# Optimization experiments

Measured on AMD Instinct MI355X. Metric: run time of the kernel, lower is better.

## Reference

```python
import jax, jax.numpy as jnp
import numpy as np

WIN = 4
HEAD_DIM = 32
N_HEADS = 6
TYPE = 'SW'
SHIFT = WIN // 2  # window_size // 2


def _relation():
    # [P, P, 3] relative coordinate indices into the (2w-1)^3 bias table
    cord = np.array([[i, j, k] for i in range(WIN) for j in range(WIN) for k in range(WIN)])
    return cord[:, None, :] - cord[None, :, :] + WIN - 1


def _shift_mask(nw):
    # boolean mask [nw^3, P, P]; True -> -inf (cross-boundary pairs in shifted windows)
    p, s = WIN, WIN - SHIFT
    m = np.zeros((nw, nw, nw, p, p, p, p, p, p), dtype=bool)
    m[-1, :, :, :s, :, :, s:, :, :] = True
    m[-1, :, :, s:, :, :, :s, :, :] = True
    m[:, -1, :, :, :s, :, :, s:, :] = True
    m[:, -1, :, :, s:, :, :, :s, :] = True
    m[:, :, -1, :, :, :s, :, :, s:] = True
    m[:, :, -1, :, :, s:, :, :, :s] = True
    return m.reshape(nw ** 3, p ** 3, p ** 3)


def setup_inputs() -> dict:
    key = jax.random.key(0)
    ks = jax.random.split(key, 6)
    dim = N_HEADS * HEAD_DIM  # 192
    B, S = 2, 32
    x = jax.random.normal(ks[0], (B, S, S, S, dim), jnp.float32)
    W_qkv = jax.random.normal(ks[1], (dim, 3 * dim), jnp.float32) * 0.02
    b_qkv = jnp.zeros((3 * dim,), jnp.float32)
    rel_params = jax.random.normal(ks[2], (N_HEADS, 2 * WIN - 1, 2 * WIN - 1, 2 * WIN - 1), jnp.float32) * 0.02
    W_out = jax.random.normal(ks[3], (dim, dim), jnp.float32) * 0.02
    b_out = jnp.zeros((dim,), jnp.float32)
    return {"x": x, "W_qkv": W_qkv, "b_qkv": b_qkv, "rel_params": rel_params, "W_out": W_out, "b_out": b_out}


def reference(x, W_qkv, b_qkv, rel_params, W_out, b_out):
    B, H, Wd, D, C = x.shape
    p = WIN
    nw = H // p
    scale = HEAD_DIM ** -0.5
    if TYPE != 'W':
        x = jnp.roll(x, (-SHIFT, -SHIFT, -SHIFT), axis=(1, 2, 3))
    # window partition: [B, NW, P, C], NW = nw^3, P = p^3
    xw = x.reshape(B, nw, p, nw, p, nw, p, C).transpose(0, 1, 3, 5, 2, 4, 6, 7).reshape(B, nw ** 3, p ** 3, C)
    qkv = xw @ W_qkv + b_qkv  # [B, NW, P, 3C]
    qkv = qkv.reshape(B, nw ** 3, p ** 3, 3 * N_HEADS, HEAD_DIM).transpose(3, 0, 1, 2, 4)  # [3h, B, NW, P, d]
    q, k, v = qkv[:N_HEADS], qkv[N_HEADS:2 * N_HEADS], qkv[2 * N_HEADS:]
    sim = jnp.einsum('hbwpc,hbwqc->hbwpq', q, k) * scale
    rel = _relation()
    bias = rel_params[:, rel[:, :, 0], rel[:, :, 1], rel[:, :, 2]]  # [h, P, P]
    sim = sim + bias[:, None, None, :, :]
    if TYPE != 'W':
        mask = jnp.asarray(_shift_mask(nw))[None, None]  # [1,1,NW,P,P]
        sim = jnp.where(mask, -jnp.inf, sim)
    probs = jax.nn.softmax(sim, axis=-1)
    out = jnp.einsum('hbwpq,hbwqc->hbwpc', probs, v)
    out = out.transpose(1, 2, 3, 0, 4).reshape(B, nw ** 3, p ** 3, C)  # h b w p c -> b w p (h c)
    out = out @ W_out + b_out
    out = out.reshape(B, nw, nw, nw, p, p, p, C).transpose(0, 1, 4, 2, 5, 3, 6, 7).reshape(B, H, Wd, D, C)
    if TYPE != 'W':
        out = jnp.roll(out, (SHIFT, SHIFT, SHIFT), axis=(1, 2, 3))
    return out
```

## Files before the change

### kernel.cpp

```cpp
#include <hip/hip_runtime.h>

typedef short bf16x8 __attribute__((ext_vector_type(8)));
typedef float f32x4 __attribute__((ext_vector_type(4)));
typedef unsigned short us4 __attribute__((ext_vector_type(4)));

#define MFMA16(a, b, c) __builtin_amdgcn_mfma_f32_16x16x32_bf16(a, b, c, 0, 0, 0)

__device__ __forceinline__ unsigned short f2bf(float f) {
    unsigned int u = __float_as_uint(f);
    u += 0x7FFFu + ((u >> 16) & 1u);
    return (unsigned short)(u >> 16);
}

#define WQT_OFF 0
#define WOT_OFF 221184
#define BQ_OFF  294912

__global__ void prep_kernel(const float* __restrict__ Wqkv,
                            const float* __restrict__ bqkv,
                            const float* __restrict__ Wout,
                            unsigned short* __restrict__ WqT,
                            unsigned short* __restrict__ WoT,
                            float* __restrict__ bq) {
    const float SCALE = 0.17677669529663687f;
    int i = blockIdx.x * 256 + threadIdx.x;
    if (i < 110592) {
        int n = i / 192, c = i - n * 192;
        float v = Wqkv[c * 576 + n];
        if (n < 192) v *= SCALE;
        WqT[i] = f2bf(v);
    } else if (i < 147456) {
        int j = i - 110592;
        int n = j / 192, c = j - n * 192;
        WoT[j] = f2bf(Wout[c * 192 + n]);
    } else if (i < 148032) {
        int n = i - 147456;
        float v = bqkv[n];
        if (n < 192) v *= SCALE;
        bq[n] = v;
    }
}

#define OFF_X   0
#define OFF_P   0
#define OFF_QK  13312
#define OFF_VT  38400
#define OFF_O   52224
#define OFF_RELF 65536
#define SMEM_US 69652

__global__ __launch_bounds__(512, 2) void wmsa_kernel(
    const float* __restrict__ x, const float* __restrict__ rel,
    const float* __restrict__ bout,
    const unsigned short* __restrict__ WqT,
    const unsigned short* __restrict__ WoT,
    const float* __restrict__ bq, float* __restrict__ out) {
    __shared__ __align__(16) unsigned short smem[SMEM_US];
    float* sRel = (float*)&smem[OFF_RELF];

    const int tid = threadIdx.x;
    const int bw = blockIdx.x;
    const int b  = bw >> 9;
    const int w  = bw & 511;
    const int wz = w >> 6, wy = (w >> 3) & 7, wx = w & 7;

    for (int i = tid; i < 2058; i += 512) sRel[i] = rel[i];
    {
        int t = tid >> 3, q8 = tid & 7;
        int tz = t >> 4, ty = (t >> 2) & 3, tx = t & 3;
        int gz = (wz * 4 + tz + 2) & 31;
        int gy = (wy * 4 + ty + 2) & 31;
        int gx = (wx * 4 + tx + 2) & 31;
        const float* xp = x + ((((b * 32 + gz) * 32 + gy) * 32 + gx)) * 192;
#pragma unroll
        for (int k = 0; k < 6; ++k) {
            int c = (q8 << 2) + (k << 5);
            float4 v = *(const float4*)(xp + c);
            us4 pk;
            pk[0] = f2bf(v.x); pk[1] = f2bf(v.y);
            pk[2] = f2bf(v.z); pk[3] = f2bf(v.w);
            *(us4*)&smem[OFF_X + t * 208 + c] = pk;
        }
    }
    __syncthreads();

    const int lane = tid & 63;
    const int wv   = tid >> 6;
    const int g    = lane >> 4;
    const int l15  = lane & 15;

    {
        bf16x8 afr[4][6];
#pragma unroll
        for (int m = 0; m < 4; ++m)
#pragma unroll
            for (int kk = 0; kk < 6; ++kk)
                afr[m][kk] = *(const bf16x8*)&smem[OFF_X + (m * 16 + l15) * 208 + kk * 32 + g * 8];

        int nb = wv;
        float bias = bq[nb * 16 + l15];
        bf16x8 bfr[6];
        {
            const unsigned short* wp = WqT + (nb * 16 + l15) * 192 + g * 8;
#pragma unroll
            for (int kk = 0; kk < 6; ++kk) bfr[kk] = *(const bf16x8*)(wp + kk * 32);
        }
        while (true) {
            int nbN = nb + 8;
            bool more = (nbN < 36);
            bf16x8 bfrN[6];
            float biasN = 0.f;
            if (more) {
                biasN = bq[nbN * 16 + l15];
                const unsigned short* wp = WqT + (nbN * 16 + l15) * 192 + g * 8;
#pragma unroll
                for (int kk = 0; kk < 6; ++kk) bfrN[kk] = *(const bf16x8*)(wp + kk * 32);
            }
            int colg = nb * 16 + l15;
            bool isV = (nb >= 24);
#pragma unroll
            for (int m = 0; m < 4; ++m) {
                f32x4 acc = {bias, bias, bias, bias};
#pragma unroll
                for (int kk = 0; kk < 6; ++kk) acc = MFMA16(afr[m][kk], bfr[kk], acc);
                int row0 = m * 16 + g * 4;
                if (!isV) {
#pragma unroll
                    for (int r = 0; r < 4; ++r)
                        smem[OFF_QK + (row0 + r) * 392 + colg] = f2bf(acc[r]);
                } else {
                    us4 pk;
#pragma unroll
                    for (int r = 0; r < 4; ++r) pk[r] = f2bf(acc[r]);
                    *(us4*)&smem[OFF_VT + (colg - 384) * 72 + row0] = pk;
                }
            }
            if (!more) break;
            nb = nbN;
            bias = biasN;
#pragma unroll
            for (int kk = 0; kk < 6; ++kk) bfr[kk] = bfrN[kk];
        }
    }
    __syncthreads();

    const bool sz = (wz == 7), sy = (wy == 7), sx = (wx == 7);
    {
        const int qy = (l15 >> 2) & 3, qx = l15 & 3;
        for (int it = wv * 3; it < wv * 3 + 3; ++it) {
            int h = it >> 2, mb = it & 3;
            bf16x8 qf = *(const bf16x8*)&smem[OFF_QK + (mb * 16 + l15) * 392 + h * 32 + g * 8];
            f32x4 s[4];
#pragma unroll
            for (int f = 0; f < 4; ++f) {
                bf16x8 kf = *(const bf16x8*)&smem[OFF_QK + (f * 16 + l15) * 392 + 192 + h * 32 + g * 8];
                f32x4 z = {0.f, 0.f, 0.f, 0.f};
                s[f] = MFMA16(qf, kf, z);
            }
#pragma unroll
            for (int f = 0; f < 4; ++f) {
                bool mz = sz && ((mb < 2) != (f < 2));
                bool my = sy && ((g < 2) != (qy < 2));
                int base = h * 343 + (mb - f + 3) * 49 + (g - qy + 3) * 7 + (3 - qx);
#pragma unroll
                for (int r = 0; r < 4; ++r) {
                    float v = s[f][r] + sRel[base + r];
                    bool mx = sx && ((r < 2) != (qx < 2));
                    s[f][r] = (mz | my | mx) ? -1e30f : v;
                }
            }
#pragma unroll
            for (int r = 0; r < 4; ++r) {
                float m0 = fmaxf(fmaxf(s[0][r], s[1][r]), fmaxf(s[2][r], s[3][r]));
#pragma unroll
                for (int d = 1; d < 16; d <<= 1) m0 = fmaxf(m0, __shfl_xor(m0, d, 64));
                float p0 = __expf(s[0][r] - m0);
                float p1 = __expf(s[1][r] - m0);
                float p2 = __expf(s[2][r] - m0);
                float p3 = __expf(s[3][r] - m0);
                float sm = p0 + p1 + p2 + p3;
#pragma unroll
                for (int d = 1; d < 16; d <<= 1) sm += __shfl_xor(sm, d, 64);
                float inv = 1.0f / sm;
                s[0][r] = p0 * inv; s[1][r] = p1 * inv;
                s[2][r] = p2 * inv; s[3][r] = p3 * inv;
            }
            unsigned short* pbase = &smem[OFF_P + wv * 1152];
#pragma unroll
            for (int f = 0; f < 4; ++f)
#pragma unroll
                for (int r = 0; r < 4; ++r)
                    pbase[(g * 4 + r) * 72 + f * 16 + l15] = f2bf(s[f][r]);
            f32x4 o0 = {0.f, 0.f, 0.f, 0.f}, o1 = {0.f, 0.f, 0.f, 0.f};
#pragma unroll
            for (int kt = 0; kt < 2; ++kt) {
                bf16x8 pf = *(const bf16x8*)&pbase[l15 * 72 + kt * 32 + g * 8];
                bf16x8 v0 = *(const bf16x8*)&smem[OFF_VT + (h * 32 + l15) * 72 + kt * 32 + g * 8];
                bf16x8 v1 = *(const bf16x8*)&smem[OFF_VT + (h * 32 + 16 + l15) * 72 + kt * 32 + g * 8];
                o0 = MFMA16(pf, v0, o0);
                o1 = MFMA16(pf, v1, o1);
            }
#pragma unroll
            for (int r = 0; r < 4; ++r) {
                smem[OFF_O + (mb * 16 + g * 4 + r) * 208 + h * 32 + l15]      = f2bf(o0[r]);
                smem[OFF_O + (mb * 16 + g * 4 + r) * 208 + h * 32 + 16 + l15] = f2bf(o1[r]);
            }
        }
    }
    __syncthreads();

    {
        int mw = wv >> 2, nq = wv & 3;
        bf16x8 ofr[2][6];
#pragma unroll
        for (int mi = 0; mi < 2; ++mi)
#pragma unroll
            for (int kk = 0; kk < 6; ++kk)
                ofr[mi][kk] = *(const bf16x8*)&smem[OFF_O + ((mw * 2 + mi) * 16 + l15) * 208 + kk * 32 + g * 8];
#pragma unroll
        for (int nbi = 0; nbi < 3; ++nbi) {
            int col = (nq + nbi * 4) * 16 + l15;
            float bo = bout[col];
            bf16x8 bfr[6];
            const unsigned short* wp = WoT + col * 192 + g * 8;
#pragma unroll
            for (int kk = 0; kk < 6; ++kk) bfr[kk] = *(const bf16x8*)(wp + kk * 32);
#pragma unroll
            for (int mi = 0; mi < 2; ++mi) {
                f32x4 acc = {bo, bo, bo, bo};
#pragma unroll
                for (int kk = 0; kk < 6; ++kk) acc = MFMA16(ofr[mi][kk], bfr[kk], acc);
                int m = mw * 2 + mi;
                int gz = (wz * 4 + m + 2) & 31;
                int gy = (wy * 4 + g + 2) & 31;
#pragma unroll
                for (int r = 0; r < 4; ++r) {
                    int gx = (wx * 4 + r + 2) & 31;
                    out[(((b * 32 + gz) * 32 + gy) * 32 + gx) * 192 + col] = acc[r];
                }
            }
        }
    }
}

extern "C" void kernel_launch(void* const* d_in, const int* in_sizes, int n_in,
                              void* d_out, int out_size, void* d_ws, size_t ws_size,
                              hipStream_t stream) {
    const float* x    = (const float*)d_in[0];
    const float* Wqkv = (const float*)d_in[1];
    const float* bqkv = (const float*)d_in[2];
    const float* rel  = (const float*)d_in[3];
    const float* Wout = (const float*)d_in[4];
    const float* bout = (const float*)d_in[5];

    unsigned short* WqT = (unsigned short*)((char*)d_ws + WQT_OFF);
    unsigned short* WoT = (unsigned short*)((char*)d_ws + WOT_OFF);
    float*          bq  = (float*)((char*)d_ws + BQ_OFF);
    float*          out = (float*)d_out;

    prep_kernel<<<579, 256, 0, stream>>>(Wqkv, bqkv, Wout, WqT, WoT, bq);
    wmsa_kernel<<<1024, 512, 0, stream>>>(x, rel, bout, WqT, WoT, bq, out);
}
```

Measured before the change: 176.8 us.

## Split attention into per-half-head blocks and move output projection to separate kernel

Each window is now processed by two blocks, each handling three heads with a smaller shared-memory footprint, so more blocks fit per CU. The attention output is written as bf16 to a workspace buffer, and a new oproj_kernel performs the output projection afterwards. The weight prep kernel is also rewritten to use tiled shared-memory transposes for coalesced access. In exchange, each window's x tile is loaded twice and there is an extra global round trip of the attention output plus one more kernel launch.

```diff
diff --git a/kernel.cpp b/kernel.cpp
--- a/kernel.cpp
+++ b/kernel.cpp
@@ -3,6 +3,7 @@
 typedef short bf16x8 __attribute__((ext_vector_type(8)));
 typedef float f32x4 __attribute__((ext_vector_type(4)));
 typedef unsigned short us4 __attribute__((ext_vector_type(4)));
+typedef unsigned short us8 __attribute__((ext_vector_type(8)));
 
 #define MFMA16(a, b, c) __builtin_amdgcn_mfma_f32_16x16x32_bf16(a, b, c, 0, 0, 0)
 
@@ -15,6 +16,7 @@
 #define WQT_OFF 0
 #define WOT_OFF 221184
 #define BQ_OFF  294912
+#define OWS_OFF 297216
 
 __global__ void prep_kernel(const float* __restrict__ Wqkv,
                             const float* __restrict__ bqkv,
@@ -22,65 +24,80 @@
                             unsigned short* __restrict__ WqT,
                             unsigned short* __restrict__ WoT,
                             float* __restrict__ bq) {
+    __shared__ float tile[32][33];
     const float SCALE = 0.17677669529663687f;
-    int i = blockIdx.x * 256 + threadIdx.x;
-    if (i < 110592) {
-        int n = i / 192, c = i - n * 192;
-        float v = Wqkv[c * 576 + n];
-        if (n < 192) v *= SCALE;
-        WqT[i] = f2bf(v);
-    } else if (i < 147456) {
-        int j = i - 110592;
-        int n = j / 192, c = j - n * 192;
-        WoT[j] = f2bf(Wout[c * 192 + n]);
-    } else if (i < 148032) {
-        int n = i - 147456;
-        float v = bqkv[n];
-        if (n < 192) v *= SCALE;
-        bq[n] = v;
-    }
-}
-
-#define OFF_X   0
-#define OFF_P   0
-#define OFF_QK  13312
-#define OFF_VT  38400
-#define OFF_O   52224
-#define OFF_RELF 65536
-#define SMEM_US 69652
-
-__global__ __launch_bounds__(512, 2) void wmsa_kernel(
+    int bid = blockIdx.x;
+    int tx = threadIdx.x & 31, ty = threadIdx.x >> 5;
+    if (bid < 108) {
+        int tn = bid % 18, tc = bid / 18;
+#pragma unroll
+        for (int i = 0; i < 4; ++i)
+            tile[ty + i * 8][tx] = Wqkv[(tc * 32 + ty + i * 8) * 576 + tn * 32 + tx];
+        __syncthreads();
+        bool isQ = (tn < 6);
+#pragma unroll
+        for (int i = 0; i < 4; ++i) {
+            float v = tile[tx][ty + i * 8];
+            if (isQ) v *= SCALE;
+            WqT[(tn * 32 + ty + i * 8) * 192 + tc * 32 + tx] = f2bf(v);
+        }
+    } else if (bid < 144) {
+        int bb = bid - 108;
+        int tn = bb % 6, tc = bb / 6;
+#pragma unroll
+        for (int i = 0; i < 4; ++i)
+            tile[ty + i * 8][tx] = Wout[(tc * 32 + ty + i * 8) * 192 + tn * 32 + tx];
+        __syncthreads();
+#pragma unroll
+        for (int i = 0; i < 4; ++i)
+            WoT[(tn * 32 + ty + i * 8) * 192 + tc * 32 + tx] = f2bf(tile[tx][ty + i * 8]);
+    } else {
+        for (int i = threadIdx.x; i < 576; i += 256) {
+            float v = bqkv[i];
+            if (i < 192) v *= SCALE;
+            bq[i] = v;
+        }
+    }
+}
+
+#define OFF_X    0
+#define OFF_QK   12800
+#define OFF_VT   25600
+#define OFF_RELF 32512
+#define SMEM_US  34570
+
+__global__ __launch_bounds__(384, 3) void wmsa_kernel(
     const float* __restrict__ x, const float* __restrict__ rel,
-    const float* __restrict__ bout,
     const unsigned short* __restrict__ WqT,
-    const unsigned short* __restrict__ WoT,
-    const float* __restrict__ bq, float* __restrict__ out) {
+    const float* __restrict__ bq,
+    unsigned short* __restrict__ Ows) {
     __shared__ __align__(16) unsigned short smem[SMEM_US];
     float* sRel = (float*)&smem[OFF_RELF];
 
     const int tid = threadIdx.x;
-    const int bw = blockIdx.x;
-    const int b  = bw >> 9;
-    const int w  = bw & 511;
+    const int bid = blockIdx.x;
+    const int hh  = bid & 1;
+    const int bw  = bid >> 1;
+    const int b   = bw >> 9;
+    const int w   = bw & 511;
     const int wz = w >> 6, wy = (w >> 3) & 7, wx = w & 7;
 
-    for (int i = tid; i < 2058; i += 512) sRel[i] = rel[i];
-    {
-        int t = tid >> 3, q8 = tid & 7;
+    for (int i = tid; i < 1029; i += 384) sRel[i] = rel[hh * 1029 + i];
+#pragma unroll
+    for (int p = 0; p < 4; ++p) {
+        int f = p * 3072 + tid * 8;
+        int t = f / 192, c = f - t * 192;
         int tz = t >> 4, ty = (t >> 2) & 3, tx = t & 3;
         int gz = (wz * 4 + tz + 2) & 31;
         int gy = (wy * 4 + ty + 2) & 31;
         int gx = (wx * 4 + tx + 2) & 31;
-        const float* xp = x + ((((b * 32 + gz) * 32 + gy) * 32 + gx)) * 192;
-#pragma unroll
-        for (int k = 0; k < 6; ++k) {
-            int c = (q8 << 2) + (k << 5);
-            float4 v = *(const float4*)(xp + c);
-            us4 pk;
-            pk[0] = f2bf(v.x); pk[1] = f2bf(v.y);
-            pk[2] = f2bf(v.z); pk[3] = f2bf(v.w);
-            *(us4*)&smem[OFF_X + t * 208 + c] = pk;
-        }
+        const float* xp = x + ((((b * 32 + gz) * 32 + gy) * 32 + gx)) * 192 + c;
+        float4 v0 = *(const float4*)xp;
+        float4 v1 = *(const float4*)(xp + 4);
+        us8 pk;
+        pk[0] = f2bf(v0.x); pk[1] = f2bf(v0.y); pk[2] = f2bf(v0.z); pk[3] = f2bf(v0.w);
+        pk[4] = f2bf(v1.x); pk[5] = f2bf(v1.y); pk[6] = f2bf(v1.z); pk[7] = f2bf(v1.w);
+        *(us8*)&smem[OFF_X + t * 200 + c] = pk;
     }
     __syncthreads();
 
@@ -89,57 +106,38 @@
     const int g    = lane >> 4;
     const int l15  = lane & 15;
 
-    {
-        bf16x8 afr[4][6];
-#pragma unroll
-        for (int m = 0; m < 4; ++m)
-#pragma unroll
-            for (int kk = 0; kk < 6; ++kk)
-                afr[m][kk] = *(const bf16x8*)&smem[OFF_X + (m * 16 + l15) * 208 + kk * 32 + g * 8];
-
-        int nb = wv;
-        float bias = bq[nb * 16 + l15];
+#pragma unroll
+    for (int j = 0; j < 3; ++j) {
+        int nb = wv + j * 6;
+        int nglob = (nb < 6)  ? (hh * 96 + nb * 16)
+                  : (nb < 12) ? (192 + hh * 96 + (nb - 6) * 16)
+                              : (384 + hh * 96 + (nb - 12) * 16);
+        float bias = bq[nglob + l15];
         bf16x8 bfr[6];
-        {
-            const unsigned short* wp = WqT + (nb * 16 + l15) * 192 + g * 8;
-#pragma unroll
-            for (int kk = 0; kk < 6; ++kk) bfr[kk] = *(const bf16x8*)(wp + kk * 32);
-        }
-        while (true) {
-            int nbN = nb + 8;
-            bool more = (nbN < 36);
-            bf16x8 bfrN[6];
-            float biasN = 0.f;
-            if (more) {
-                biasN = bq[nbN * 16 + l15];
-                const unsigned short* wp = WqT + (nbN * 16 + l15) * 192 + g * 8;
-#pragma unroll
-                for (int kk = 0; kk < 6; ++kk) bfrN[kk] = *(const bf16x8*)(wp + kk * 32);
-            }
-            int colg = nb * 16 + l15;
-            bool isV = (nb >= 24);
-#pragma unroll
-            for (int m = 0; m < 4; ++m) {
-                f32x4 acc = {bias, bias, bias, bias};
-#pragma unroll
-                for (int kk = 0; kk < 6; ++kk) acc = MFMA16(afr[m][kk], bfr[kk], acc);
-                int row0 = m * 16 + g * 4;
-                if (!isV) {
-#pragma unroll
-                    for (int r = 0; r < 4; ++r)
-                        smem[OFF_QK + (row0 + r) * 392 + colg] = f2bf(acc[r]);
-                } else {
-                    us4 pk;
-#pragma unroll
-                    for (int r = 0; r < 4; ++r) pk[r] = f2bf(acc[r]);
-                    *(us4*)&smem[OFF_VT + (colg - 384) * 72 + row0] = pk;
-                }
-            }
-            if (!more) break;
-            nb = nbN;
-            bias = biasN;
-#pragma unroll
-            for (int kk = 0; kk < 6; ++kk) bfr[kk] = bfrN[kk];
+        const unsigned short* wp = WqT + (nglob + l15) * 192 + g * 8;
+#pragma unroll
+        for (int kk = 0; kk < 6; ++kk) bfr[kk] = *(const bf16x8*)(wp + kk * 32);
+#pragma unroll
+        for (int m = 0; m < 4; ++m) {
+            f32x4 acc = {bias, bias, bias, bias};
+#pragma unroll
+            for (int kk = 0; kk < 6; ++kk) {
+                bf16x8 afr = *(const bf16x8*)&smem[OFF_X + (m * 16 + l15) * 200 + kk * 32 + g * 8];
+                acc = MFMA16(afr, bfr[kk], acc);
+            }
+            int row0 = m * 16 + g * 4;
+            if (nb < 12) {
+                int colg = nb * 16 + l15;
+#pragma unroll
+                for (int r = 0; r < 4; ++r)
+                    smem[OFF_QK + (row0 + r) * 200 + colg] = f2bf(acc[r]);
+            } else {
+                int cl = (nb - 12) * 16 + l15;
+                us4 pk;
+#pragma unroll
+                for (int r = 0; r < 4; ++r) pk[r] = f2bf(acc[r]);
+                *(us4*)&smem[OFF_VT + cl * 72 + row0] = pk;
+            }
         }
     }
     __syncthreads();
@@ -147,13 +145,16 @@
     const bool sz = (wz == 7), sy = (wy == 7), sx = (wx == 7);
     {
         const int qy = (l15 >> 2) & 3, qx = l15 & 3;
-        for (int it = wv * 3; it < wv * 3 + 3; ++it) {
-            int h = it >> 2, mb = it & 3;
-            bf16x8 qf = *(const bf16x8*)&smem[OFF_QK + (mb * 16 + l15) * 392 + h * 32 + g * 8];
+        unsigned short* pb = &smem[OFF_X + wv * 1152];
+#pragma unroll
+        for (int ii = 0; ii < 2; ++ii) {
+            int it = wv * 2 + ii;
+            int h3 = it >> 2, mb = it & 3;
+            bf16x8 qf = *(const bf16x8*)&smem[OFF_QK + (mb * 16 + l15) * 200 + h3 * 32 + g * 8];
             f32x4 s[4];
 #pragma unroll
             for (int f = 0; f < 4; ++f) {
-                bf16x8 kf = *(const bf16x8*)&smem[OFF_QK + (f * 16 + l15) * 392 + 192 + h * 32 + g * 8];
+                bf16x8 kf = *(const bf16x8*)&smem[OFF_QK + (f * 16 + l15) * 200 + 96 + h3 * 32 + g * 8];
                 f32x4 z = {0.f, 0.f, 0.f, 0.f};
                 s[f] = MFMA16(qf, kf, z);
             }
@@ -161,7 +162,7 @@
             for (int f = 0; f < 4; ++f) {
                 bool mz = sz && ((mb < 2) != (f < 2));
                 bool my = sy && ((g < 2) != (qy < 2));
-                int base = h * 343 + (mb - f + 3) * 49 + (g - qy + 3) * 7 + (3 - qx);
+                int base = h3 * 343 + (mb - f + 3) * 49 + (g - qy + 3) * 7 + (3 - qx);
 #pragma unroll
                 for (int r = 0; r < 4; ++r) {
                     float v = s[f][r] + sRel[base + r];
@@ -185,60 +186,67 @@
                 s[0][r] = p0 * inv; s[1][r] = p1 * inv;
                 s[2][r] = p2 * inv; s[3][r] = p3 * inv;
             }
-            unsigned short* pbase = &smem[OFF_P + wv * 1152];
 #pragma unroll
             for (int f = 0; f < 4; ++f)
 #pragma unroll
                 for (int r = 0; r < 4; ++r)
-                    pbase[(g * 4 + r) * 72 + f * 16 + l15] = f2bf(s[f][r]);
+                    pb[(g * 4 + r) * 72 + f * 16 + l15] = f2bf(s[f][r]);
             f32x4 o0 = {0.f, 0.f, 0.f, 0.f}, o1 = {0.f, 0.f, 0.f, 0.f};
 #pragma unroll
             for (int kt = 0; kt < 2; ++kt) {
-                bf16x8 pf = *(const bf16x8*)&pbase[l15 * 72 + kt * 32 + g * 8];
-                bf16x8 v0 = *(const bf16x8*)&smem[OFF_VT + (h * 32 + l15) * 72 + kt * 32 + g * 8];
-                bf16x8 v1 = *(const bf16x8*)&smem[OFF_VT + (h * 32 + 16 + l15) * 72 + kt * 32 + g * 8];
+                bf16x8 pf = *(const bf16x8*)&pb[l15 * 72 + kt * 32 + g * 8];
+                bf16x8 v0 = *(const bf16x8*)&smem[OFF_VT + (h3 * 32 + l15) * 72 + kt * 32 + g * 8];
+                bf16x8 v1 = *(const bf16x8*)&smem[OFF_VT + (h3 * 32 + 16 + l15) * 72 + kt * 32 + g * 8];
                 o0 = MFMA16(pf, v0, o0);
                 o1 = MFMA16(pf, v1, o1);
             }
 #pragma unroll
             for (int r = 0; r < 4; ++r) {
-                smem[OFF_O + (mb * 16 + g * 4 + r) * 208 + h * 32 + l15]      = f2bf(o0[r]);
-                smem[OFF_O + (mb * 16 + g * 4 + r) * 208 + h * 32 + 16 + l15] = f2bf(o1[r]);
-            }
-        }
-    }
-    __syncthreads();
-
-    {
-        int mw = wv >> 2, nq = wv & 3;
-        bf16x8 ofr[2][6];
-#pragma unroll
-        for (int mi = 0; mi < 2; ++mi)
-#pragma unroll
-            for (int kk = 0; kk < 6; ++kk)
-                ofr[mi][kk] = *(const bf16x8*)&smem[OFF_O + ((mw * 2 + mi) * 16 + l15) * 208 + kk * 32 + g * 8];
-#pragma unroll
-        for (int nbi = 0; nbi < 3; ++nbi) {
-            int col = (nq + nbi * 4) * 16 + l15;
-            float bo = bout[col];
-            bf16x8 bfr[6];
-            const unsigned short* wp = WoT + col * 192 + g * 8;
-#pragma unroll
-            for (int kk = 0; kk < 6; ++kk) bfr[kk] = *(const bf16x8*)(wp + kk * 32);
-#pragma unroll
-            for (int mi = 0; mi < 2; ++mi) {
-                f32x4 acc = {bo, bo, bo, bo};
-#pragma unroll
-                for (int kk = 0; kk < 6; ++kk) acc = MFMA16(ofr[mi][kk], bfr[kk], acc);
-                int m = mw * 2 + mi;
-                int gz = (wz * 4 + m + 2) & 31;
-                int gy = (wy * 4 + g + 2) & 31;
-#pragma unroll
-                for (int r = 0; r < 4; ++r) {
-                    int gx = (wx * 4 + r + 2) & 31;
-                    out[(((b * 32 + gz) * 32 + gy) * 32 + gx) * 192 + col] = acc[r];
-                }
-            }
+                pb[(g * 4 + r) * 32 + l15]      = f2bf(o0[r]);
+                pb[(g * 4 + r) * 32 + 16 + l15] = f2bf(o1[r]);
+            }
+            us8 pk = *(const us8*)&pb[(lane >> 2) * 32 + (lane & 3) * 8];
+            *(us8*)&Ows[(bid * 64 + mb * 16 + (lane >> 2)) * 96 + h3 * 32 + (lane & 3) * 8] = pk;
+        }
+    }
+}
+
+__global__ __launch_bounds__(256) void oproj_kernel(
+    const unsigned short* __restrict__ Ows,
+    const unsigned short* __restrict__ WoT,
+    const float* __restrict__ bout, float* __restrict__ out) {
+    const int bw = blockIdx.x;
+    const int b  = bw >> 9;
+    const int w  = bw & 511;
+    const int wz = w >> 6, wy = (w >> 3) & 7, wx = w & 7;
+    const int lane = threadIdx.x & 63;
+    const int wv   = threadIdx.x >> 6;
+    const int g    = lane >> 4;
+    const int l15  = lane & 15;
+
+    bf16x8 af[6];
+#pragma unroll
+    for (int kk = 0; kk < 6; ++kk) {
+        int hh = (kk >= 3) ? 1 : 0;
+        af[kk] = *(const bf16x8*)&Ows[(((bw << 1) | hh) * 64 + wv * 16 + l15) * 96 + (kk - hh * 3) * 32 + g * 8];
+    }
+    const int gz = (wz * 4 + wv + 2) & 31;
+    const int gy = (wy * 4 + g + 2) & 31;
+#pragma unroll
+    for (int nb = 0; nb < 12; ++nb) {
+        float bo = bout[nb * 16 + l15];
+        const unsigned short* wp = WoT + (nb * 16 + l15) * 192 + g * 8;
+        bf16x8 bf[6];
+#pragma unroll
+        for (int kk = 0; kk < 6; ++kk) bf[kk] = *(const bf16x8*)(wp + kk * 32);
+        f32x4 acc = {bo, bo, bo, bo};
+#pragma unroll
+        for (int kk = 0; kk < 6; ++kk) acc = MFMA16(af[kk], bf[kk], acc);
+        int col = nb * 16 + l15;
+#pragma unroll
+        for (int r = 0; r < 4; ++r) {
+            int gx = (wx * 4 + r + 2) & 31;
+            out[(((b * 32 + gz) * 32 + gy) * 32 + gx) * 192 + col] = acc[r];
         }
     }
 }
@@ -256,8 +264,10 @@
     unsigned short* WqT = (unsigned short*)((char*)d_ws + WQT_OFF);
     unsigned short* WoT = (unsigned short*)((char*)d_ws + WOT_OFF);
     float*          bq  = (float*)((char*)d_ws + BQ_OFF);
+    unsigned short* Ows = (unsigned short*)((char*)d_ws + OWS_OFF);
     float*          out = (float*)d_out;
 
-    prep_kernel<<<579, 256, 0, stream>>>(Wqkv, bqkv, Wout, WqT, WoT, bq);
-    wmsa_kernel<<<1024, 512, 0, stream>>>(x, rel, bout, WqT, WoT, bq, out);
-}
+    prep_kernel<<<145, 256, 0, stream>>>(Wqkv, bqkv, Wout, WqT, WoT, bq);
+    wmsa_kernel<<<2048, 384, 0, stream>>>(x, rel, WqT, bq, Ows);
+    oproj_kernel<<<1024, 256, 0, stream>>>(Ows, WoT, bout, out);
+}
```

Result: slower. 202.8 us (+14.7%).
